# Kernel optimization log

Hardware: AMD Instinct MI355X
Metric: run time of the kernel (lower is better)

## Reference

```python
import jax, jax.numpy as jnp
import numpy as np
from jax import lax

# --- db4 filters (pywt convention) ---
DEC_LO = np.array([-0.010597401784997278, 0.032883011666982945,
                   0.030841381835986965, -0.18703481171888114,
                   -0.02798376941698385, 0.6308807679295904,
                   0.7148465705525415, 0.23037781330885523], dtype=np.float32)
L = len(DEC_LO)
DEC_HI = np.array([((-1.0) ** (k + 1)) * DEC_LO[L - 1 - k] for k in range(L)], dtype=np.float32)
REC_LO = DEC_LO[::-1].copy()  # orthogonal reconstruction filters
REC_HI = DEC_HI[::-1].copy()


def _afb1d(x, axis):
    """Analysis filter bank along `axis` (2 or 3) of (B,C,H,W), symmetric pad, stride 2.
    Matches pytorch_wavelets afb1d with mode='symmetric'."""
    N = x.shape[axis]
    out = (N + L - 1) // 2            # pywt dwt_coeff_len for symmetric mode
    p = 2 * (out - 1) - N + L
    pads = [(0, 0)] * 4
    pads[axis] = (p // 2, (p + 1) // 2)
    xp = jnp.pad(x, pads, mode='symmetric')
    B, C = x.shape[0], x.shape[1]
    xr = xp.reshape(B * C, 1, xp.shape[2], xp.shape[3])
    # conv2d is correlation -> use time-reversed decomposition filters
    f = jnp.asarray(np.stack([DEC_LO[::-1], DEC_HI[::-1]]))  # (2, L)
    if axis == 3:
        kern = f[:, None, None, :]; strides = (1, 2)
    else:
        kern = f[:, None, :, None]; strides = (2, 1)
    y = lax.conv_general_dilated(xr, kern, strides, 'VALID',
                                 dimension_numbers=('NCHW', 'OIHW', 'NCHW'))
    lo = y[:, 0].reshape(B, C, y.shape[2], y.shape[3])
    hi = y[:, 1].reshape(B, C, y.shape[2], y.shape[3])
    return lo, hi


def dwt2(x):
    # pytorch_wavelets AFB2D: filter dim=3 (width) first, then dim=2 (height)
    lox, hix = _afb1d(x, 3)
    ll, lh = _afb1d(lox, 2)   # lh = (x-low, y-high)  -> highs[0]
    hl, hh = _afb1d(hix, 2)   # hl = (x-high, y-low) -> highs[1]; hh -> highs[2]
    return ll, lh, hl, hh


def _sfb1d(lo, hi, axis):
    """Synthesis filter bank: conv_transpose(stride=2, padding=L-2) expressed as a
    zero-dilated correlation with the flipped reconstruction filter."""
    B, C = lo.shape[0], lo.shape[1]

    def up(x, g):
        xr = x.reshape(B * C, 1, x.shape[2], x.shape[3])
        gf = jnp.asarray(np.asarray(g)[::-1].copy())
        if axis == 3:
            kern = gf[None, None, None, :]; lhs = (1, 2); pad = ((0, 0), (1, 1))
        else:
            kern = gf[None, None, :, None]; lhs = (2, 1); pad = ((1, 1), (0, 0))
        y = lax.conv_general_dilated(xr, kern, (1, 1), pad, lhs_dilation=lhs,
                                     dimension_numbers=('NCHW', 'OIHW', 'NCHW'))
        return y.reshape(B, C, y.shape[2], y.shape[3])

    return up(lo, REC_LO) + up(hi, REC_HI)


def idwt2(ll, lh, hl, hh):
    lo = _sfb1d(ll, lh, 2)
    hi = _sfb1d(hl, hh, 2)
    return _sfb1d(lo, hi, 3)


def mul2d(x, w):
    # per-mode channel mixing: (B,Ci,x,y) x (Ci,Co,x,y) -> (B,Co,x,y)
    return jnp.einsum('bixy,ioxy->boxy', x, w)


def wno_block(h, wb, cw, cb):
    ll, lh, hl, hh = dwt2(h)
    x1 = idwt2(mul2d(ll, wb[0]), mul2d(lh, wb[1]), mul2d(hl, wb[2]), mul2d(hh, wb[3]))
    x2 = jnp.einsum('bixy,oi->boxy', h, cw) + cb[None, :, None, None]  # 1x1 conv
    return jax.nn.relu(x1 + x2)


def setup_inputs() -> dict:
    key = jax.random.key(0)
    ks = jax.random.split(key, 10)
    B, S, W, M = 32, 64, 64, 35  # M = (64 + 8 - 1) // 2 for db4, level 1
    scale = 1.0 / (W * W)
    return {
        'x': jax.random.normal(ks[0], (B, S, S, 3), jnp.float32),
        'fc0_w': jax.random.normal(ks[1], (5, W), jnp.float32) * 0.1,
        'fc0_b': jnp.zeros((W,), jnp.float32),
        'wno_w': jax.random.uniform(ks[2], (4, 4, W, W, M, M), jnp.float32) * scale,
        'conv_w': jax.random.normal(ks[3], (4, W, W), jnp.float32) * 0.05,
        'conv_b': jnp.zeros((4, W), jnp.float32),
        'fc1_w': jax.random.normal(ks[4], (W, 256), jnp.float32) * 0.05,
        'fc1_b': jnp.zeros((256,), jnp.float32),
        'fc2_w': jax.random.normal(ks[5], (256, 1), jnp.float32) * 0.05,
        'fc2_b': jnp.zeros((1,), jnp.float32),
    }


def reference(x, fc0_w, fc0_b, wno_w, conv_w, conv_b, fc1_w, fc1_b, fc2_w, fc2_b):
    B, Sx, Sy, _ = x.shape
    gx = jnp.linspace(0.0, 1.0, Sx, dtype=x.dtype)
    gy = jnp.linspace(0.0, 1.0, Sy, dtype=x.dtype)
    gxb, gyb = jnp.broadcast_arrays(gx[:, None], gy[None, :])
    grid = jnp.broadcast_to(jnp.stack([gxb, gyb], -1)[None], (B, Sx, Sy, 2))
    h = jnp.concatenate([x, grid], axis=-1) @ fc0_w + fc0_b
    h = h.transpose(0, 3, 1, 2)  # (B, width, Sx, Sy)
    for i in range(4):  # only conv0..conv3 / w0..w3 are used in the original forward
        h = wno_block(h, wno_w[i], conv_w[i], conv_b[i])
    h = h.transpose(0, 2, 3, 1)
    h = jax.nn.relu(h @ fc1_w + fc1_b)
    return h @ fc2_w + fc2_b
```

## Files before the change

kernel.cpp:

```cpp
#include <hip/hip_runtime.h>
#include <hip/hip_bf16.h>

#define DL_INIT {-0.010597401784997278f, 0.032883011666982945f, 0.030841381835986965f, \
  -0.18703481171888114f, -0.02798376941698385f, 0.6308807679295904f, \
  0.7148465705525415f, 0.23037781330885523f}
#define DH_INIT {-0.23037781330885523f, 0.7148465705525415f, -0.6308807679295904f, \
  -0.02798376941698385f, 0.18703481171888114f, 0.030841381835986965f, \
  -0.032883011666982945f, -0.010597401784997278f}

#define SP 1232
#define PLANE 2523136

using bf16x8 = __attribute__((ext_vector_type(8))) short;
using f32x4  = __attribute__((ext_vector_type(4))) float;

__device__ __forceinline__ short f2bf(float f) {
    unsigned u = __builtin_bit_cast(unsigned, f);
    u += 0x7FFFu + ((u >> 16) & 1u);
    return (short)(u >> 16);
}

__global__ __launch_bounds__(256) void k_fc0(const float* __restrict__ x,
    const float* __restrict__ w, const float* __restrict__ bias,
    float* __restrict__ h)
{
    int g = blockIdx.x * 256 + threadIdx.x;
    int b = g >> 18, c = (g >> 12) & 63, sx = (g >> 6) & 63, sy = g & 63;
    const float* xp = x + ((b * 64 + sx) * 64 + sy) * 3;
    float f3 = (float)sx / 63.0f, f4 = (float)sy / 63.0f;
    float acc = bias[c];
    acc = fmaf(xp[0], w[0 * 64 + c], acc);
    acc = fmaf(xp[1], w[1 * 64 + c], acc);
    acc = fmaf(xp[2], w[2 * 64 + c], acc);
    acc = fmaf(f3,    w[3 * 64 + c], acc);
    acc = fmaf(f4,    w[4 * 64 + c], acc);
    h[g] = acc;
}

__global__ __launch_bounds__(256) void k_dwt(const float* __restrict__ h,
    float* __restrict__ s)
{
    constexpr float DL[8] = DL_INIT;
    constexpr float DH[8] = DH_INIT;
    __shared__ float xs[4096];
    __shared__ float tlo[2240];
    __shared__ float thi[2240];
    int bc = blockIdx.x, t = threadIdx.x;
    const float* hp = h + bc * 4096;
    #pragma unroll
    for (int k = 0; k < 16; ++k) xs[t + k * 256] = hp[t + k * 256];
    __syncthreads();
    for (int u = t; u < 2240; u += 256) {
        int sx = u / 35, oy = u - sx * 35;
        int y0 = 2 * oy + 1;
        float al = 0.f, ah = 0.f;
        #pragma unroll
        for (int j = 0; j < 8; ++j) {
            int yy = y0 - j;
            yy = (yy < 0) ? (-1 - yy) : yy;
            yy = (yy > 63) ? (127 - yy) : yy;
            float v = xs[sx * 64 + yy];
            al = fmaf(DL[j], v, al);
            ah = fmaf(DH[j], v, ah);
        }
        tlo[u] = al; thi[u] = ah;
    }
    __syncthreads();
    float* s0 = s + bc * SP;
    for (int u = t; u < 1225; u += 256) {
        int ox = u / 35, oy = u - ox * 35;
        int x0 = 2 * ox + 1;
        float a_ll = 0.f, a_lh = 0.f, a_hl = 0.f, a_hh = 0.f;
        #pragma unroll
        for (int j = 0; j < 8; ++j) {
            int xx = x0 - j;
            xx = (xx < 0) ? (-1 - xx) : xx;
            xx = (xx > 63) ? (127 - xx) : xx;
            float vl = tlo[xx * 35 + oy];
            float vh = thi[xx * 35 + oy];
            a_ll = fmaf(DL[j], vl, a_ll);
            a_lh = fmaf(DH[j], vl, a_lh);
            a_hl = fmaf(DL[j], vh, a_hl);
            a_hh = fmaf(DH[j], vh, a_hh);
        }
        s0[u]             = a_ll;
        s0[PLANE + u]     = a_lh;
        s0[2 * PLANE + u] = a_hl;
        s0[3 * PLANE + u] = a_hh;
    }
}

__global__ __launch_bounds__(128) void k_mul2d(const float* __restrict__ sIn,
    const float* __restrict__ W, float* __restrict__ mOut)
{
    int raw = blockIdx.x;
    int xcd = raw & 7, kk = raw >> 3;
    int sid = (xcd < 4) ? (xcd * 39 + kk) : (156 + (xcd - 4) * 38 + kk);
    int tile = sid >> 1, og = sid & 1;
    int z = blockIdx.y;
    int p0 = tile * 8;
    const float* in = sIn + (size_t)z * PLANE;
    const float* w  = W   + (size_t)z * 5017600;
    float* out = mOut + (size_t)z * PLANE;
    int t = threadIdx.x;
    int p = t & 7, wg = t >> 3;
    int oA = og * 32 + wg * 2;
    int pp = min(p0 + p, 1224);
    float a0[32], a1[32];
    #pragma unroll
    for (int b = 0; b < 32; ++b) { a0[b] = 0.f; a1[b] = 0.f; }
    __shared__ float inp[4 * 8 * 34];

    const float* src[8];
    int dst[8];
    #pragma unroll
    for (int k = 0; k < 8; ++k) {
        int e = t + k * 128;
        int pl = e & 7, ii = (e >> 3) & 3, b = e >> 5;
        int gp = min(p0 + pl, 1224);
        src[k] = in + (b * 64 + ii) * SP + gp;
        dst[k] = (ii * 8 + pl) * 34 + b;
    }
    float r[8];
    #pragma unroll
    for (int k = 0; k < 8; ++k) r[k] = src[k][0];

    for (int ic = 0; ic < 64; ic += 4) {
        __syncthreads();
        #pragma unroll
        for (int k = 0; k < 8; ++k) inp[dst[k]] = r[k];
        __syncthreads();
        if (ic < 60) {
            #pragma unroll
            for (int k = 0; k < 8; ++k) r[k] = src[k][(ic + 4) * SP];
        }
        #pragma unroll
        for (int ii = 0; ii < 4; ++ii) {
            int i = ic + ii;
            float w0 = w[(i * 64 + oA) * 1225 + pp];
            float w1 = w[(i * 64 + oA + 1) * 1225 + pp];
            const float2* ip = reinterpret_cast<const float2*>(&inp[(ii * 8 + p) * 34]);
            #pragma unroll
            for (int bq = 0; bq < 16; ++bq) {
                float2 v = ip[bq];
                a0[bq * 2]     = fmaf(v.x, w0, a0[bq * 2]);
                a1[bq * 2]     = fmaf(v.x, w1, a1[bq * 2]);
                a0[bq * 2 + 1] = fmaf(v.y, w0, a0[bq * 2 + 1]);
                a1[bq * 2 + 1] = fmaf(v.y, w1, a1[bq * 2 + 1]);
            }
        }
    }
    if (p0 + p < 1225) {
        #pragma unroll
        for (int b = 0; b < 32; ++b) {
            out[(b * 64 + oA) * SP + p0 + p]     = a0[b];
            out[(b * 64 + oA + 1) * SP + p0 + p] = a1[b];
        }
    }
}

__global__ __launch_bounds__(256) void k_idwt_col(const float* __restrict__ m,
    float* __restrict__ uLo, float* __restrict__ uHi)
{
    constexpr float DL[8] = DL_INIT;
    constexpr float DH[8] = DH_INIT;
    int bc = blockIdx.x, z = blockIdx.y, t = threadIdx.x;
    const float* lo = m + (size_t)(z * 2) * PLANE + bc * SP;
    const float* hi = m + (size_t)(z * 2 + 1) * PLANE + bc * SP;
    float* uo = (z ? uHi : uLo) + bc * 2240;
    for (int u = t; u < 2240; u += 256) {
        int n = u / 35, oy = u - n * 35;
        int q = n & 1, mm = n >> 1;
        float cl0 = q ? DL[0] : DL[1], cl1 = q ? DL[2] : DL[3];
        float cl2 = q ? DL[4] : DL[5], cl3 = q ? DL[6] : DL[7];
        float ch0 = q ? DH[0] : DH[1], ch1 = q ? DH[2] : DH[3];
        float ch2 = q ? DH[4] : DH[5], ch3 = q ? DH[6] : DH[7];
        int base = mm * 35 + oy;
        float a = cl0 * lo[base];
        a = fmaf(cl1, lo[base + 35], a);
        a = fmaf(cl2, lo[base + 70], a);
        a = fmaf(cl3, lo[base + 105], a);
        a = fmaf(ch0, hi[base], a);
        a = fmaf(ch1, hi[base + 35], a);
        a = fmaf(ch2, hi[base + 70], a);
        a = fmaf(ch3, hi[base + 105], a);
        uo[u] = a;
    }
}

__global__ __launch_bounds__(256) void k_pconv_idwt(const float* __restrict__ h,
    const float* __restrict__ uLo, const float* __restrict__ uHi,
    const float* __restrict__ cw, const float* __restrict__ cb,
    float* __restrict__ hOut)
{
    constexpr float DL[8] = DL_INIT;
    constexpr float DH[8] = DH_INIT;
    __shared__ float cwt[4096];
    __shared__ float hs[64][128];
    int t = threadIdx.x;
    #pragma unroll
    for (int k = 0; k < 16; ++k) {
        int e = t + k * 256;
        cwt[e] = cw[(e & 63) * 64 + (e >> 6)];
    }
    int px0g = blockIdx.x * 128;
    int b = px0g >> 12, pxl0 = px0g & 4095;
    const float* hb = h + ((size_t)b << 18) + pxl0;
    #pragma unroll
    for (int kk = 0; kk < 8; ++kk) {
        int c = kk * 8 + (t >> 5), col = (t & 31) * 4;
        *reinterpret_cast<float4*>(&hs[c][col]) =
            *reinterpret_cast<const float4*>(&hb[(c << 12) + col]);
    }
    __syncthreads();
    int p2 = t & 63, og = t >> 6;
    int o0 = og * 16;
    float acc0[16], acc1[16];
    #pragma unroll
    for (int oo = 0; oo < 16; ++oo) { acc0[oo] = cb[o0 + oo]; acc1[oo] = acc0[oo]; }
    for (int i = 0; i < 64; ++i) {
        float2 hv = *reinterpret_cast<const float2*>(&hs[i][p2 * 2]);
        const float4* wv = reinterpret_cast<const float4*>(&cwt[i * 64 + o0]);
        #pragma unroll
        for (int q4 = 0; q4 < 4; ++q4) {
            float4 wq = wv[q4];
            acc0[q4 * 4 + 0] = fmaf(hv.x, wq.x, acc0[q4 * 4 + 0]);
            acc1[q4 * 4 + 0] = fmaf(hv.y, wq.x, acc1[q4 * 4 + 0]);
            acc0[q4 * 4 + 1] = fmaf(hv.x, wq.y, acc0[q4 * 4 + 1]);
            acc1[q4 * 4 + 1] = fmaf(hv.y, wq.y, acc1[q4 * 4 + 1]);
            acc0[q4 * 4 + 2] = fmaf(hv.x, wq.z, acc0[q4 * 4 + 2]);
            acc1[q4 * 4 + 2] = fmaf(hv.y, wq.z, acc1[q4 * 4 + 2]);
            acc0[q4 * 4 + 3] = fmaf(hv.x, wq.w, acc0[q4 * 4 + 3]);
            acc1[q4 * 4 + 3] = fmaf(hv.y, wq.w, acc1[q4 * 4 + 3]);
        }
    }
    int pxe = pxl0 + 2 * p2;
    int sx = pxe >> 6, sy = pxe & 63;
    int mm = sy >> 1;
    const float* lp = uLo + (((size_t)(b << 6) + o0) * 2240) + sx * 35 + mm;
    const float* hq = uHi + (((size_t)(b << 6) + o0) * 2240) + sx * 35 + mm;
    float* op = hOut + ((size_t)b << 18) + pxe;
    #pragma unroll
    for (int oo = 0; oo < 16; ++oo) {
        const float* l = lp + oo * 2240;
        const float* g = hq + oo * 2240;
        float l0 = l[0], l1 = l[1], l2 = l[2], l3 = l[3];
        float g0 = g[0], g1 = g[1], g2 = g[2], g3 = g[3];
        float xe = DL[1] * l0;
        xe = fmaf(DL[3], l1, xe); xe = fmaf(DL[5], l2, xe); xe = fmaf(DL[7], l3, xe);
        xe = fmaf(DH[1], g0, xe); xe = fmaf(DH[3], g1, xe);
        xe = fmaf(DH[5], g2, xe); xe = fmaf(DH[7], g3, xe);
        float xo = DL[0] * l0;
        xo = fmaf(DL[2], l1, xo); xo = fmaf(DL[4], l2, xo); xo = fmaf(DL[6], l3, xo);
        xo = fmaf(DH[0], g0, xo); xo = fmaf(DH[2], g1, xo);
        xo = fmaf(DH[4], g2, xo); xo = fmaf(DH[6], g3, xo);
        float2 r;
        r.x = fmaxf(acc0[oo] + xe, 0.f);
        r.y = fmaxf(acc1[oo] + xo, 0.f);
        *reinterpret_cast<float2*>(&op[(o0 + oo) << 12]) = r;
    }
}

__global__ __launch_bounds__(256) void k_fc_final(const float* __restrict__ h,
    const float* __restrict__ w1, const float* __restrict__ b1,
    const float* __restrict__ w2, const float* __restrict__ b2,
    float* __restrict__ out)
{
    int t = threadIdx.x;
    int l = t & 63, wid = t >> 6;
    int lr = l & 15, lg = l >> 4;
    float part[2][4];
    #pragma unroll
    for (int it = 0; it < 2; ++it)
        #pragma unroll
        for (int r = 0; r < 4; ++r) part[it][r] = 0.f;

    int pxbase = blockIdx.x * 128 + wid * 32;

    for (int nh = 0; nh < 2; ++nh) {
        bf16x8 Bf[8][2];
        #pragma unroll
        for (int tt = 0; tt < 8; ++tt) {
            #pragma unroll
            for (int kh = 0; kh < 2; ++kh) {
                const float* wp = w1 + (kh * 32 + lg * 8) * 256 + nh * 128 + tt * 16 + lr;
                bf16x8 f;
                #pragma unroll
                for (int e = 0; e < 8; ++e) f[e] = f2bf(wp[e * 256]);
                Bf[tt][kh] = f;
            }
        }
        #pragma unroll
        for (int it = 0; it < 2; ++it) {
            int pxg = pxbase + it * 16;
            int b = pxg >> 12, pxl = pxg & 4095;
            const float* hp = h + ((size_t)b << 18) + pxl + lr + (size_t)(lg * 8) * 4096;
            bf16x8 Af[2];
            #pragma unroll
            for (int kh = 0; kh < 2; ++kh) {
                bf16x8 f;
                #pragma unroll
                for (int e = 0; e < 8; ++e)
                    f[e] = f2bf(hp[(size_t)(kh * 32 + e) * 4096]);
                Af[kh] = f;
            }
            #pragma unroll
            for (int tt = 0; tt < 8; ++tt) {
                f32x4 acc = {0.f, 0.f, 0.f, 0.f};
                acc = __builtin_amdgcn_mfma_f32_16x16x32_bf16(Af[0], Bf[tt][0], acc, 0, 0, 0);
                acc = __builtin_amdgcn_mfma_f32_16x16x32_bf16(Af[1], Bf[tt][1], acc, 0, 0, 0);
                int n = nh * 128 + tt * 16 + lr;
                float bj = b1[n], wj = w2[n];
                #pragma unroll
                for (int r = 0; r < 4; ++r)
                    part[it][r] = fmaf(fmaxf(acc[r] + bj, 0.f), wj, part[it][r]);
            }
        }
    }
    float bb = b2[0];
    #pragma unroll
    for (int it = 0; it < 2; ++it) {
        #pragma unroll
        for (int r = 0; r < 4; ++r) {
            float v = part[it][r];
            v += __shfl_xor(v, 1);
            v += __shfl_xor(v, 2);
            v += __shfl_xor(v, 4);
            v += __shfl_xor(v, 8);
            if (lr == 0) out[pxbase + it * 16 + lg * 4 + r] = v + bb;
        }
    }
}

extern "C" void kernel_launch(void* const* d_in, const int* in_sizes, int n_in,
                              void* d_out, int out_size, void* d_ws, size_t ws_size,
                              hipStream_t stream)
{
    const float* x     = (const float*)d_in[0];
    const float* fc0w  = (const float*)d_in[1];
    const float* fc0b  = (const float*)d_in[2];
    const float* wno   = (const float*)d_in[3];
    const float* convw = (const float*)d_in[4];
    const float* convb = (const float*)d_in[5];
    const float* fc1w  = (const float*)d_in[6];
    const float* fc1b  = (const float*)d_in[7];
    const float* fc2w  = (const float*)d_in[8];
    const float* fc2b  = (const float*)d_in[9];
    (void)in_sizes; (void)n_in; (void)out_size; (void)ws_size;

    float* ws  = (float*)d_ws;
    float* hA  = ws;
    float* hB  = hA + 8388608;
    float* sU  = hB + 8388608;
    float* mB  = sU + 4 * (size_t)PLANE;
    float* uLo = sU;
    float* uHi = sU + 4587520;

    k_fc0<<<32768, 256, 0, stream>>>(x, fc0w, fc0b, hA);

    float* hin = hA;
    float* hout = hB;
    for (int blk = 0; blk < 4; ++blk) {
        k_dwt<<<2048, 256, 0, stream>>>(hin, sU);
        k_mul2d<<<dim3(308, 4), 128, 0, stream>>>(sU, wno + (size_t)blk * 20070400, mB);
        k_idwt_col<<<dim3(2048, 2), 256, 0, stream>>>(mB, uLo, uHi);
        k_pconv_idwt<<<1024, 256, 0, stream>>>(hin, uLo, uHi,
                                               convw + blk * 4096, convb + blk * 64, hout);
        float* tmp = hin; hin = hout; hout = tmp;
    }

    k_fc_final<<<1024, 256, 0, stream>>>(hin, fc1w, fc1b, fc2w, fc2b,
                                         (float*)d_out);
}
```

Measured before the change: 556.0 us.

## Store all intermediate activations and wavelet buffers in fp16

Every intermediate buffer (hidden activations, DWT coefficients, spectral-multiply outputs, column-IDWT outputs) changes from fp32 to fp16 storage. Arithmetic still runs in fp32 after conversion. The final MLP switches its MFMA from bf16 to f16. This halves global memory traffic for the activation-heavy kernels, at the cost of reduced precision and fp16 range limits on intermediates. The wno weights, which are large, stay fp32.

Result: faster. 488.9 us, median of 2 (-12.1%).

```diff
diff --git a/kernel.cpp b/kernel.cpp
--- a/kernel.cpp
+++ b/kernel.cpp
@@ -1,5 +1,6 @@
 #include <hip/hip_runtime.h>
 #include <hip/hip_bf16.h>
+#include <hip/hip_fp16.h>
 
 #define DL_INIT {-0.010597401784997278f, 0.032883011666982945f, 0.030841381835986965f, \
   -0.18703481171888114f, -0.02798376941698385f, 0.6308807679295904f, \
@@ -11,18 +12,14 @@
 #define SP 1232
 #define PLANE 2523136
 
-using bf16x8 = __attribute__((ext_vector_type(8))) short;
-using f32x4  = __attribute__((ext_vector_type(4))) float;
-
-__device__ __forceinline__ short f2bf(float f) {
-    unsigned u = __builtin_bit_cast(unsigned, f);
-    u += 0x7FFFu + ((u >> 16) & 1u);
-    return (short)(u >> 16);
-}
+typedef _Float16 half_t;
+typedef _Float16 half8 __attribute__((ext_vector_type(8)));
+typedef _Float16 half2v __attribute__((ext_vector_type(2)));
+using f32x4 = __attribute__((ext_vector_type(4))) float;
 
 __global__ __launch_bounds__(256) void k_fc0(const float* __restrict__ x,
     const float* __restrict__ w, const float* __restrict__ bias,
-    float* __restrict__ h)
+    half_t* __restrict__ h)
 {
     int g = blockIdx.x * 256 + threadIdx.x;
     int b = g >> 18, c = (g >> 12) & 63, sx = (g >> 6) & 63, sy = g & 63;
@@ -34,11 +31,11 @@
     acc = fmaf(xp[2], w[2 * 64 + c], acc);
     acc = fmaf(f3,    w[3 * 64 + c], acc);
     acc = fmaf(f4,    w[4 * 64 + c], acc);
-    h[g] = acc;
-}
-
-__global__ __launch_bounds__(256) void k_dwt(const float* __restrict__ h,
-    float* __restrict__ s)
+    h[g] = (half_t)acc;
+}
+
+__global__ __launch_bounds__(256) void k_dwt(const half_t* __restrict__ h,
+    half_t* __restrict__ s)
 {
     constexpr float DL[8] = DL_INIT;
     constexpr float DH[8] = DH_INIT;
@@ -46,9 +43,9 @@
     __shared__ float tlo[2240];
     __shared__ float thi[2240];
     int bc = blockIdx.x, t = threadIdx.x;
-    const float* hp = h + bc * 4096;
-    #pragma unroll
-    for (int k = 0; k < 16; ++k) xs[t + k * 256] = hp[t + k * 256];
+    const half_t* hp = h + bc * 4096;
+    #pragma unroll
+    for (int k = 0; k < 16; ++k) xs[t + k * 256] = (float)hp[t + k * 256];
     __syncthreads();
     for (int u = t; u < 2240; u += 256) {
         int sx = u / 35, oy = u - sx * 35;
@@ -66,7 +63,7 @@
         tlo[u] = al; thi[u] = ah;
     }
     __syncthreads();
-    float* s0 = s + bc * SP;
+    half_t* s0 = s + bc * SP;
     for (int u = t; u < 1225; u += 256) {
         int ox = u / 35, oy = u - ox * 35;
         int x0 = 2 * ox + 1;
@@ -83,15 +80,15 @@
             a_hl = fmaf(DL[j], vh, a_hl);
             a_hh = fmaf(DH[j], vh, a_hh);
         }
-        s0[u]             = a_ll;
-        s0[PLANE + u]     = a_lh;
-        s0[2 * PLANE + u] = a_hl;
-        s0[3 * PLANE + u] = a_hh;
-    }
-}
-
-__global__ __launch_bounds__(128) void k_mul2d(const float* __restrict__ sIn,
-    const float* __restrict__ W, float* __restrict__ mOut)
+        s0[u]             = (half_t)a_ll;
+        s0[PLANE + u]     = (half_t)a_lh;
+        s0[2 * PLANE + u] = (half_t)a_hl;
+        s0[3 * PLANE + u] = (half_t)a_hh;
+    }
+}
+
+__global__ __launch_bounds__(128) void k_mul2d(const half_t* __restrict__ sIn,
+    const float* __restrict__ W, half_t* __restrict__ mOut)
 {
     int raw = blockIdx.x;
     int xcd = raw & 7, kk = raw >> 3;
@@ -99,9 +96,9 @@
     int tile = sid >> 1, og = sid & 1;
     int z = blockIdx.y;
     int p0 = tile * 8;
-    const float* in = sIn + (size_t)z * PLANE;
-    const float* w  = W   + (size_t)z * 5017600;
-    float* out = mOut + (size_t)z * PLANE;
+    const half_t* in = sIn + (size_t)z * PLANE;
+    const float* w   = W   + (size_t)z * 5017600;
+    half_t* out = mOut + (size_t)z * PLANE;
     int t = threadIdx.x;
     int p = t & 7, wg = t >> 3;
     int oA = og * 32 + wg * 2;
@@ -111,7 +108,7 @@
     for (int b = 0; b < 32; ++b) { a0[b] = 0.f; a1[b] = 0.f; }
     __shared__ float inp[4 * 8 * 34];
 
-    const float* src[8];
+    const half_t* src[8];
     int dst[8];
     #pragma unroll
     for (int k = 0; k < 8; ++k) {
@@ -123,7 +120,7 @@
     }
     float r[8];
     #pragma unroll
-    for (int k = 0; k < 8; ++k) r[k] = src[k][0];
+    for (int k = 0; k < 8; ++k) r[k] = (float)src[k][0];
 
     for (int ic = 0; ic < 64; ic += 4) {
         __syncthreads();
@@ -132,7 +129,7 @@
         __syncthreads();
         if (ic < 60) {
             #pragma unroll
-            for (int k = 0; k < 8; ++k) r[k] = src[k][(ic + 4) * SP];
+            for (int k = 0; k < 8; ++k) r[k] = (float)src[k][(ic + 4) * SP];
         }
         #pragma unroll
         for (int ii = 0; ii < 4; ++ii) {
@@ -153,21 +150,21 @@
     if (p0 + p < 1225) {
         #pragma unroll
         for (int b = 0; b < 32; ++b) {
-            out[(b * 64 + oA) * SP + p0 + p]     = a0[b];
-            out[(b * 64 + oA + 1) * SP + p0 + p] = a1[b];
-        }
-    }
-}
-
-__global__ __launch_bounds__(256) void k_idwt_col(const float* __restrict__ m,
-    float* __restrict__ uLo, float* __restrict__ uHi)
+            out[(b * 64 + oA) * SP + p0 + p]     = (half_t)a0[b];
+            out[(b * 64 + oA + 1) * SP + p0 + p] = (half_t)a1[b];
+        }
+    }
+}
+
+__global__ __launch_bounds__(256) void k_idwt_col(const half_t* __restrict__ m,
+    half_t* __restrict__ uLo, half_t* __restrict__ uHi)
 {
     constexpr float DL[8] = DL_INIT;
     constexpr float DH[8] = DH_INIT;
     int bc = blockIdx.x, z = blockIdx.y, t = threadIdx.x;
-    const float* lo = m + (size_t)(z * 2) * PLANE + bc * SP;
-    const float* hi = m + (size_t)(z * 2 + 1) * PLANE + bc * SP;
-    float* uo = (z ? uHi : uLo) + bc * 2240;
+    const half_t* lo = m + (size_t)(z * 2) * PLANE + bc * SP;
+    const half_t* hi = m + (size_t)(z * 2 + 1) * PLANE + bc * SP;
+    half_t* uo = (z ? uHi : uLo) + bc * 2240;
     for (int u = t; u < 2240; u += 256) {
         int n = u / 35, oy = u - n * 35;
         int q = n & 1, mm = n >> 1;
@@ -176,27 +173,27 @@
         float ch0 = q ? DH[0] : DH[1], ch1 = q ? DH[2] : DH[3];
         float ch2 = q ? DH[4] : DH[5], ch3 = q ? DH[6] : DH[7];
         int base = mm * 35 + oy;
-        float a = cl0 * lo[base];
-        a = fmaf(cl1, lo[base + 35], a);
-        a = fmaf(cl2, lo[base + 70], a);
-        a = fmaf(cl3, lo[base + 105], a);
-        a = fmaf(ch0, hi[base], a);
-        a = fmaf(ch1, hi[base + 35], a);
-        a = fmaf(ch2, hi[base + 70], a);
-        a = fmaf(ch3, hi[base + 105], a);
-        uo[u] = a;
-    }
-}
-
-__global__ __launch_bounds__(256) void k_pconv_idwt(const float* __restrict__ h,
-    const float* __restrict__ uLo, const float* __restrict__ uHi,
+        float a = cl0 * (float)lo[base];
+        a = fmaf(cl1, (float)lo[base + 35], a);
+        a = fmaf(cl2, (float)lo[base + 70], a);
+        a = fmaf(cl3, (float)lo[base + 105], a);
+        a = fmaf(ch0, (float)hi[base], a);
+        a = fmaf(ch1, (float)hi[base + 35], a);
+        a = fmaf(ch2, (float)hi[base + 70], a);
+        a = fmaf(ch3, (float)hi[base + 105], a);
+        uo[u] = (half_t)a;
+    }
+}
+
+__global__ __launch_bounds__(256) void k_pconv_idwt(const half_t* __restrict__ h,
+    const half_t* __restrict__ uLo, const half_t* __restrict__ uHi,
     const float* __restrict__ cw, const float* __restrict__ cb,
-    float* __restrict__ hOut)
+    half_t* __restrict__ hOut)
 {
     constexpr float DL[8] = DL_INIT;
     constexpr float DH[8] = DH_INIT;
     __shared__ float cwt[4096];
-    __shared__ float hs[64][128];
+    __shared__ half_t hs[64][128];
     int t = threadIdx.x;
     #pragma unroll
     for (int k = 0; k < 16; ++k) {
@@ -205,12 +202,13 @@
     }
     int px0g = blockIdx.x * 128;
     int b = px0g >> 12, pxl0 = px0g & 4095;
-    const float* hb = h + ((size_t)b << 18) + pxl0;
-    #pragma unroll
-    for (int kk = 0; kk < 8; ++kk) {
-        int c = kk * 8 + (t >> 5), col = (t & 31) * 4;
-        *reinterpret_cast<float4*>(&hs[c][col]) =
-            *reinterpret_cast<const float4*>(&hb[(c << 12) + col]);
+    const half_t* hb = h + ((size_t)b << 18) + pxl0;
+    #pragma unroll
+    for (int k = 0; k < 4; ++k) {
+        int e = t + k * 256;
+        int c = e >> 4, col = (e & 15) * 8;
+        *reinterpret_cast<half8*>(&hs[c][col]) =
+            *reinterpret_cast<const half8*>(&hb[(c << 12) + col]);
     }
     __syncthreads();
     int p2 = t & 63, og = t >> 6;
@@ -219,33 +217,34 @@
     #pragma unroll
     for (int oo = 0; oo < 16; ++oo) { acc0[oo] = cb[o0 + oo]; acc1[oo] = acc0[oo]; }
     for (int i = 0; i < 64; ++i) {
-        float2 hv = *reinterpret_cast<const float2*>(&hs[i][p2 * 2]);
+        half2v hraw = *reinterpret_cast<const half2v*>(&hs[i][p2 * 2]);
+        float hvx = (float)hraw[0], hvy = (float)hraw[1];
         const float4* wv = reinterpret_cast<const float4*>(&cwt[i * 64 + o0]);
         #pragma unroll
         for (int q4 = 0; q4 < 4; ++q4) {
             float4 wq = wv[q4];
-            acc0[q4 * 4 + 0] = fmaf(hv.x, wq.x, acc0[q4 * 4 + 0]);
-            acc1[q4 * 4 + 0] = fmaf(hv.y, wq.x, acc1[q4 * 4 + 0]);
-            acc0[q4 * 4 + 1] = fmaf(hv.x, wq.y, acc0[q4 * 4 + 1]);
-            acc1[q4 * 4 + 1] = fmaf(hv.y, wq.y, acc1[q4 * 4 + 1]);
-            acc0[q4 * 4 + 2] = fmaf(hv.x, wq.z, acc0[q4 * 4 + 2]);
-            acc1[q4 * 4 + 2] = fmaf(hv.y, wq.z, acc1[q4 * 4 + 2]);
-            acc0[q4 * 4 + 3] = fmaf(hv.x, wq.w, acc0[q4 * 4 + 3]);
-            acc1[q4 * 4 + 3] = fmaf(hv.y, wq.w, acc1[q4 * 4 + 3]);
+            acc0[q4 * 4 + 0] = fmaf(hvx, wq.x, acc0[q4 * 4 + 0]);
+            acc1[q4 * 4 + 0] = fmaf(hvy, wq.x, acc1[q4 * 4 + 0]);
+            acc0[q4 * 4 + 1] = fmaf(hvx, wq.y, acc0[q4 * 4 + 1]);
+            acc1[q4 * 4 + 1] = fmaf(hvy, wq.y, acc1[q4 * 4 + 1]);
+            acc0[q4 * 4 + 2] = fmaf(hvx, wq.z, acc0[q4 * 4 + 2]);
+            acc1[q4 * 4 + 2] = fmaf(hvy, wq.z, acc1[q4 * 4 + 2]);
+            acc0[q4 * 4 + 3] = fmaf(hvx, wq.w, acc0[q4 * 4 + 3]);
+            acc1[q4 * 4 + 3] = fmaf(hvy, wq.w, acc1[q4 * 4 + 3]);
         }
     }
     int pxe = pxl0 + 2 * p2;
     int sx = pxe >> 6, sy = pxe & 63;
     int mm = sy >> 1;
-    const float* lp = uLo + (((size_t)(b << 6) + o0) * 2240) + sx * 35 + mm;
-    const float* hq = uHi + (((size_t)(b << 6) + o0) * 2240) + sx * 35 + mm;
-    float* op = hOut + ((size_t)b << 18) + pxe;
+    const half_t* lp = uLo + (((size_t)(b << 6) + o0) * 2240) + sx * 35 + mm;
+    const half_t* hq = uHi + (((size_t)(b << 6) + o0) * 2240) + sx * 35 + mm;
+    half_t* op = hOut + ((size_t)b << 18) + pxe;
     #pragma unroll
     for (int oo = 0; oo < 16; ++oo) {
-        const float* l = lp + oo * 2240;
-        const float* g = hq + oo * 2240;
-        float l0 = l[0], l1 = l[1], l2 = l[2], l3 = l[3];
-        float g0 = g[0], g1 = g[1], g2 = g[2], g3 = g[3];
+        const half_t* l = lp + oo * 2240;
+        const half_t* g = hq + oo * 2240;
+        float l0 = (float)l[0], l1 = (float)l[1], l2 = (float)l[2], l3 = (float)l[3];
+        float g0 = (float)g[0], g1 = (float)g[1], g2 = (float)g[2], g3 = (float)g[3];
         float xe = DL[1] * l0;
         xe = fmaf(DL[3], l1, xe); xe = fmaf(DL[5], l2, xe); xe = fmaf(DL[7], l3, xe);
         xe = fmaf(DH[1], g0, xe); xe = fmaf(DH[3], g1, xe);
@@ -254,14 +253,14 @@
         xo = fmaf(DL[2], l1, xo); xo = fmaf(DL[4], l2, xo); xo = fmaf(DL[6], l3, xo);
         xo = fmaf(DH[0], g0, xo); xo = fmaf(DH[2], g1, xo);
         xo = fmaf(DH[4], g2, xo); xo = fmaf(DH[6], g3, xo);
-        float2 r;
-        r.x = fmaxf(acc0[oo] + xe, 0.f);
-        r.y = fmaxf(acc1[oo] + xo, 0.f);
-        *reinterpret_cast<float2*>(&op[(o0 + oo) << 12]) = r;
-    }
-}
-
-__global__ __launch_bounds__(256) void k_fc_final(const float* __restrict__ h,
+        half2v rv;
+        rv[0] = (half_t)fmaxf(acc0[oo] + xe, 0.f);
+        rv[1] = (half_t)fmaxf(acc1[oo] + xo, 0.f);
+        *reinterpret_cast<half2v*>(&op[(size_t)(o0 + oo) << 12]) = rv;
+    }
+}
+
+__global__ __launch_bounds__(256) void k_fc_final(const half_t* __restrict__ h,
     const float* __restrict__ w1, const float* __restrict__ b1,
     const float* __restrict__ w2, const float* __restrict__ b2,
     float* __restrict__ out)
@@ -278,15 +277,15 @@
     int pxbase = blockIdx.x * 128 + wid * 32;
 
     for (int nh = 0; nh < 2; ++nh) {
-        bf16x8 Bf[8][2];
+        half8 Bf[8][2];
         #pragma unroll
         for (int tt = 0; tt < 8; ++tt) {
             #pragma unroll
             for (int kh = 0; kh < 2; ++kh) {
                 const float* wp = w1 + (kh * 32 + lg * 8) * 256 + nh * 128 + tt * 16 + lr;
-                bf16x8 f;
+                half8 f;
                 #pragma unroll
-                for (int e = 0; e < 8; ++e) f[e] = f2bf(wp[e * 256]);
+                for (int e = 0; e < 8; ++e) f[e] = (half_t)wp[e * 256];
                 Bf[tt][kh] = f;
             }
         }
@@ -294,21 +293,21 @@
         for (int it = 0; it < 2; ++it) {
             int pxg = pxbase + it * 16;
             int b = pxg >> 12, pxl = pxg & 4095;
-            const float* hp = h + ((size_t)b << 18) + pxl + lr + (size_t)(lg * 8) * 4096;
-            bf16x8 Af[2];
+            const half_t* hp = h + ((size_t)b << 18) + pxl + lr + (size_t)(lg * 8) * 4096;
+            half8 Af[2];
             #pragma unroll
             for (int kh = 0; kh < 2; ++kh) {
-                bf16x8 f;
+                half8 f;
                 #pragma unroll
                 for (int e = 0; e < 8; ++e)
-                    f[e] = f2bf(hp[(size_t)(kh * 32 + e) * 4096]);
+                    f[e] = hp[(size_t)(kh * 32 + e) * 4096];
                 Af[kh] = f;
             }
             #pragma unroll
             for (int tt = 0; tt < 8; ++tt) {
                 f32x4 acc = {0.f, 0.f, 0.f, 0.f};
-                acc = __builtin_amdgcn_mfma_f32_16x16x32_bf16(Af[0], Bf[tt][0], acc, 0, 0, 0);
-                acc = __builtin_amdgcn_mfma_f32_16x16x32_bf16(Af[1], Bf[tt][1], acc, 0, 0, 0);
+                acc = __builtin_amdgcn_mfma_f32_16x16x32_f16(Af[0], Bf[tt][0], acc, 0, 0, 0);
+                acc = __builtin_amdgcn_mfma_f32_16x16x32_f16(Af[1], Bf[tt][1], acc, 0, 0, 0);
                 int n = nh * 128 + tt * 16 + lr;
                 float bj = b1[n], wj = w2[n];
                 #pragma unroll
@@ -348,25 +347,25 @@
     const float* fc2b  = (const float*)d_in[9];
     (void)in_sizes; (void)n_in; (void)out_size; (void)ws_size;
 
-    float* ws  = (float*)d_ws;
-    float* hA  = ws;
-    float* hB  = hA + 8388608;
-    float* sU  = hB + 8388608;
-    float* mB  = sU + 4 * (size_t)PLANE;
-    float* uLo = sU;
-    float* uHi = sU + 4587520;
+    half_t* ws  = (half_t*)d_ws;
+    half_t* hA  = ws;
+    half_t* hB  = hA + 8388608;
+    half_t* sU  = hB + 8388608;
+    half_t* mB  = sU + 4 * (size_t)PLANE;
+    half_t* uLo = sU;
+    half_t* uHi = sU + 4587520;
 
     k_fc0<<<32768, 256, 0, stream>>>(x, fc0w, fc0b, hA);
 
-    float* hin = hA;
-    float* hout = hB;
+    half_t* hin = hA;
+    half_t* hout = hB;
     for (int blk = 0; blk < 4; ++blk) {
         k_dwt<<<2048, 256, 0, stream>>>(hin, sU);
         k_mul2d<<<dim3(308, 4), 128, 0, stream>>>(sU, wno + (size_t)blk * 20070400, mB);
         k_idwt_col<<<dim3(2048, 2), 256, 0, stream>>>(mB, uLo, uHi);
         k_pconv_idwt<<<1024, 256, 0, stream>>>(hin, uLo, uHi,
                                                convw + blk * 4096, convb + blk * 64, hout);
-        float* tmp = hin; hin = hout; hout = tmp;
+        half_t* tmp = hin; hin = hout; hout = tmp;
     }
 
     k_fc_final<<<1024, 256, 0, stream>>>(hin, fc1w, fc1b, fc2w, fc2b,
```
